# Performance work log

Hardware: AMD Instinct MI355X
Metric: run time of the kernel (lower is better)

Reference implementation:

```python
import jax, jax.numpy as jnp
import numpy as np
import math

B, S, DIM = 2, 2048, 2048
H = 16
NOPE, ROPE = 96, 32
HD = 128          # head_dim = NOPE + ROPE
KVR, QR = 512, 1536


def _rope_tables():
    inv_freq = 1.0 / (10000.0 ** (np.arange(0, ROPE, 2, dtype=np.float32) / ROPE))  # [ROPE/2]
    t = np.arange(S, dtype=np.float32)
    freqs = np.outer(t, inv_freq)  # [S, ROPE/2]
    return jnp.asarray(np.cos(freqs)), jnp.asarray(np.sin(freqs))


def setup_inputs() -> dict:
    key = jax.random.key(0)
    ks = jax.random.split(key, 8)
    w = 0.02
    cos, sin = _rope_tables()
    return {
        "x": jax.random.normal(ks[0], (B, S, DIM), jnp.float32),
        "freqs_cos": cos,
        "freqs_sin": sin,
        "wq_down": jax.random.normal(ks[1], (DIM, QR), jnp.float32) * w,
        "wq_up": jax.random.normal(ks[2], (QR, H * HD), jnp.float32) * w,
        "wkv_down": jax.random.normal(ks[3], (DIM, KVR), jnp.float32) * w,
        "w_up_nope": jax.random.normal(ks[4], (KVR, H * NOPE), jnp.float32) * w,
        "w_up_rope": jax.random.normal(ks[5], (KVR, H * ROPE), jnp.float32) * w,
        "w_up_val": jax.random.normal(ks[6], (KVR, H * HD), jnp.float32) * w,
        "wo": jax.random.normal(ks[7], (H * HD, DIM), jnp.float32) * w,
    }


def _apply_rope(x, cos, sin):
    # x: [B, S, H, D_r]; cos/sin: [S, D_r/2]
    xr = x[..., 0::2]
    xi = x[..., 1::2]
    c = cos[None, :, None, :]
    s = sin[None, :, None, :]
    out_r = xr * c - xi * s
    out_i = xr * s + xi * c
    return jnp.stack([out_r, out_i], axis=-1).reshape(x.shape)


def reference(x, freqs_cos, freqs_sin, wq_down, wq_up, wkv_down,
              w_up_nope, w_up_rope, w_up_val, wo):
    b, s, _ = x.shape
    # Q path: low-rank down then up
    q = (x @ wq_down) @ wq_up                 # [B,S,H*HD]
    q = q.reshape(b, s, H, HD)
    q_nope, q_rope = q[..., :NOPE], q[..., NOPE:]
    q_rope = _apply_rope(q_rope, freqs_cos, freqs_sin)

    # KV path: shared latent
    kv_latent = x @ wkv_down                  # [B,S,KVR]
    k_nope = (kv_latent @ w_up_nope).reshape(b, s, H, NOPE)
    k_rope = _apply_rope((kv_latent @ w_up_rope).reshape(b, s, H, ROPE),
                         freqs_cos, freqs_sin)
    v = (kv_latent @ w_up_val).reshape(b, s, H, HD)

    q_final = jnp.concatenate([q_nope, q_rope], axis=-1)   # [B,S,H,HD]
    k_final = jnp.concatenate([k_nope, k_rope], axis=-1)

    scores = jnp.einsum("bqhd,bkhd->bhqk", q_final, k_final) / math.sqrt(HD)
    causal = jnp.tril(jnp.ones((s, s), dtype=bool))        # [S,S]
    scores = jnp.where(causal[None, None], scores, -jnp.inf)
    attn = jax.nn.softmax(scores, axis=-1)
    out = jnp.einsum("bhqk,bkhd->bqhd", attn, v).reshape(b, s, H * HD)
    return out @ wo
```

## Files before the change

### kernel.cpp

```cpp
#include <hip/hip_runtime.h>
#include <hip/hip_bf16.h>
#include <stdint.h>

#define B_    2
#define S_    2048
#define DIM_  2048
#define H_    16
#define NOPE_ 96
#define ROPE_ 32
#define HD_   128
#define KVR_  512
#define QR_   1536
#define BS_   (B_*S_)
#define NQT_  (S_/128)

typedef __bf16 bf16_t;
typedef bf16_t bf16x8 __attribute__((ext_vector_type(8)));
typedef float  f32x4  __attribute__((ext_vector_type(4)));

__device__ __forceinline__ uint16_t f2bf(float f) {
  union { float f; uint32_t u; } v; v.f = f;
  uint32_t r = (v.u + 0x7fffu + ((v.u >> 16) & 1u)) >> 16;
  return (uint16_t)r;
}
__device__ __forceinline__ float bf2f(uint16_t h) {
  union { uint32_t u; float f; } v; v.u = ((uint32_t)h) << 16;
  return v.f;
}
__device__ __forceinline__ uint32_t pk_bf16(float a, float b) {
  union { float f; uint32_t u; } x, y; x.f = a; y.f = b;
  uint32_t lo = (x.u + 0x7fffu + ((x.u >> 16) & 1u)) >> 16;
  uint32_t hi = (y.u + 0x7fffu + ((y.u >> 16) & 1u)) & 0xffff0000u;
  return hi | lo;
}

__device__ __forceinline__ void gl_lds16(const void* g, void* l) {
  __builtin_amdgcn_global_load_lds(
      (const __attribute__((address_space(1))) uint32_t*)g,
      (__attribute__((address_space(3))) uint32_t*)l, 16, 0, 0);
}

__device__ __forceinline__ void transpose_tile(const float* __restrict__ W,
                                               uint16_t* __restrict__ Wt,
                                               int K, int N, float scale, int lbid,
                                               float (*tile)[65]) {
  const int nb = N / 64;
  const int n0 = (lbid % nb) * 64, k0 = (lbid / nb) * 64;
  const int tid = threadIdx.x;
  #pragma unroll
  for (int i = 0; i < 4; i++) {
    int p = i * 256 + tid;
    int r = p >> 4, c4 = (p & 15) * 4;
    float4 v = *(const float4*)&W[(size_t)(k0 + r) * N + n0 + c4];
    tile[r][c4 + 0] = v.x; tile[r][c4 + 1] = v.y; tile[r][c4 + 2] = v.z; tile[r][c4 + 3] = v.w;
  }
  __syncthreads();
  #pragma unroll
  for (int i = 0; i < 4; i++) {
    int p = i * 256 + tid;
    int rn = p >> 4, c4 = (p & 15) * 4;
    ushort4 o;
    o.x = f2bf(tile[c4 + 0][rn] * scale); o.y = f2bf(tile[c4 + 1][rn] * scale);
    o.z = f2bf(tile[c4 + 2][rn] * scale); o.w = f2bf(tile[c4 + 3][rn] * scale);
    *(ushort4*)&Wt[(size_t)(n0 + rn) * K + k0 + c4] = o;
  }
}

#define CAST_BLKS 2048
__global__ __launch_bounds__(256) void prep_k(
    const float* __restrict__ x,
    const float* __restrict__ wqd, const float* __restrict__ wqu,
    const float* __restrict__ wkvd, const float* __restrict__ wn,
    const float* __restrict__ wr, const float* __restrict__ wv,
    const float* __restrict__ wo,
    uint16_t* __restrict__ xb, uint16_t* __restrict__ wdT,
    uint16_t* __restrict__ wquT, uint16_t* __restrict__ wkrT,
    uint16_t* __restrict__ wvT, uint16_t* __restrict__ woT, float qscale) {
  __shared__ __align__(16) float tile[64][65];
  int bid = blockIdx.x;
  const int tid = threadIdx.x;
  if (bid < CAST_BLKS) {
    #pragma unroll
    for (int p = 0; p < 4; p++) {
      int i = bid * 4096 + p * 1024 + tid * 4;
      float4 v = *(const float4*)&x[i];
      ushort4 o; o.x = f2bf(v.x); o.y = f2bf(v.y); o.z = f2bf(v.z); o.w = f2bf(v.w);
      *(ushort4*)&xb[i] = o;
    }
    return;
  }
  bid -= CAST_BLKS;
  if (bid < 768)               transpose_tile(wqd,  wdT,                        2048, 1536, 1.f,    bid, tile);
  else if ((bid -= 768) < 256) transpose_tile(wkvd, wdT + (size_t)QR_ * DIM_,   2048,  512, 1.f,    bid, tile);
  else if ((bid -= 256) < 768) transpose_tile(wqu,  wquT,                       1536, 2048, qscale, bid, tile);
  else if ((bid -= 768) < 192) transpose_tile(wn,   wkrT,                        512, 1536, 1.f,    bid, tile);
  else if ((bid -= 192) < 64)  transpose_tile(wr,   wkrT + (size_t)1536 * 512,   512,  512, 1.f,    bid, tile);
  else if ((bid -= 64) < 256)  transpose_tile(wv,   wvT,                         512, 2048, 1.f,    bid, tile);
  else                         transpose_tile(wo,   woT, 2048, 2048, 1.f, bid - 256, tile);
}
#define PREP_BLKS (CAST_BLKS + 768 + 256 + 768 + 192 + 64 + 256 + 1024)

template<int MODE>
__global__ __launch_bounds__(256) void gemm_bt(const uint16_t* __restrict__ A,
                                               const uint16_t* __restrict__ Bt,
                                               void* __restrict__ C,
                                               int M, int N, int K,
                                               int lda, int ldb, int ldc,
                                               const float* __restrict__ cos_t,
                                               const float* __restrict__ sin_t) {
  __shared__ __align__(16) uint16_t As[128][64];
  __shared__ __align__(16) uint16_t Bs[128][64];
  const int tid = threadIdx.x;
  const int wave = tid >> 6, lane = tid & 63;
  const int wm = wave & 1, wn = wave >> 1;
  const int m0 = blockIdx.y * 128, n0 = blockIdx.x * 128;
  const int fr = lane & 15, fq = lane >> 4;

  f32x4 acc[4][4] = {};

  const int srow = wave * 32 + (lane >> 3);
  const int sg   = ((lane & 7) ^ ((lane >> 3) & 7));
  const int scol = sg * 8;

  for (int k0 = 0; k0 < K; k0 += 64) {
    #pragma unroll
    for (int i = 0; i < 4; i++) {
      gl_lds16(A  + (size_t)(m0 + srow + i * 8) * lda + k0 + scol, &As[wave * 32 + i * 8][0]);
      gl_lds16(Bt + (size_t)(n0 + srow + i * 8) * ldb + k0 + scol, &Bs[wave * 32 + i * 8][0]);
    }
    __syncthreads();
    #pragma unroll
    for (int ks = 0; ks < 2; ks++) {
      bf16x8 af[4], bf[4];
      #pragma unroll
      for (int mt = 0; mt < 4; mt++) {
        int pc = (ks * 4 + fq) ^ (fr & 7);
        af[mt] = *(const bf16x8*)&As[wm * 64 + mt * 16 + fr][pc * 8];
      }
      #pragma unroll
      for (int nt = 0; nt < 4; nt++) {
        int pc = (ks * 4 + fq) ^ (fr & 7);
        bf[nt] = *(const bf16x8*)&Bs[wn * 64 + nt * 16 + fr][pc * 8];
      }
      #pragma unroll
      for (int mt = 0; mt < 4; mt++)
        #pragma unroll
        for (int nt = 0; nt < 4; nt++)
          acc[mt][nt] = __builtin_amdgcn_mfma_f32_16x16x32_bf16(af[mt], bf[nt], acc[mt][nt], 0, 0, 0);
    }
    __syncthreads();
  }
  #pragma unroll
  for (int mt = 0; mt < 4; mt++) {
    #pragma unroll
    for (int nt = 0; nt < 4; nt++) {
      #pragma unroll
      for (int r = 0; r < 4; r++) {
        int gm = m0 + wm * 64 + mt * 16 + fq * 4 + r;
        int gn = n0 + wn * 64 + nt * 16 + fr;
        float v = acc[mt][nt][r];
        if (MODE == 0) {
          ((uint16_t*)C)[(size_t)gm * ldc + gn] = f2bf(v);
        } else if (MODE == 1) {
          ((float*)C)[(size_t)gm * ldc + gn] = v;
        } else if (MODE == 2) {
          float other = __shfl_xor(v, 1);
          int d = gn & 127;
          if (d >= 96) {
            int s = gm & (S_ - 1);
            int i = (d - 96) >> 1;
            float c = cos_t[s * 16 + i], sn = sin_t[s * 16 + i];
            v = (fr & 1) ? (other * sn + v * c) : (v * c - other * sn);
          }
          ((uint16_t*)C)[(size_t)gm * ldc + gn] = f2bf(v);
        } else {
          float other = __shfl_xor(v, 1);
          int dstcol;
          if (gn < 1536) {
            int h = gn / 96;
            dstcol = h * 128 + (gn - h * 96);
          } else {
            int ln = gn - 1536;
            int h = ln >> 5, dd = ln & 31;
            int s = gm & (S_ - 1);
            float c = cos_t[s * 16 + (dd >> 1)], sn = sin_t[s * 16 + (dd >> 1)];
            v = (fr & 1) ? (other * sn + v * c) : (v * c - other * sn);
            dstcol = h * 128 + 96 + dd;
          }
          ((uint16_t*)C)[(size_t)gm * 2048 + dstcol] = f2bf(v);
        }
      }
    }
  }
}

__global__ __launch_bounds__(512) void attn_kernel(const uint16_t* __restrict__ Q,
                                                   const uint16_t* __restrict__ Kf,
                                                   const uint16_t* __restrict__ Vt,
                                                   uint16_t* __restrict__ O) {
  __shared__ __align__(16) uint16_t Ks[64][128];
  __shared__ __align__(16) uint16_t Vs[128][64];
  __shared__ __align__(16) uint16_t Ps[8][16][72];
  const int bid = blockIdx.x;
  const int qt = (NQT_ - 1) - (bid / (H_ * B_));
  const int hb = bid % (H_ * B_);
  const int h = hb >> 1, b = hb & 1;
  const int tid = threadIdx.x, wave = tid >> 6, lane = tid & 63;
  const int fr = lane & 15, fq = lane >> 4;
  const int q0 = qt * 128;
  const int qrow = q0 + wave * 16;

  bf16x8 qf[4];
  const uint16_t* qbase = Q + (size_t)(b * S_ + qrow + fr) * (H_ * HD_) + h * HD_ + fq * 8;
  #pragma unroll
  for (int s4 = 0; s4 < 4; s4++) qf[s4] = *(const bf16x8*)(qbase + s4 * 32);

  float l_s = 0.f;
  f32x4 oacc[8] = {};

  const int ksrow_lo = wave * 4 + (lane >> 4);
  const int kg_chunk0 = (lane & 15);
  const int vsrow_lo = wave * 8 + (lane >> 3);
  const int vg_chunk = (lane & 7) ^ ((lane >> 3) & 7);

  const int nkt = 2 * qt + 2;
  for (int kt = 0; kt < nkt; kt++) {
    #pragma unroll
    for (int i = 0; i < 2; i++) {
      int row = i * 32 + ksrow_lo;
      int g = kg_chunk0 ^ (row & 15);
      gl_lds16(Kf + (size_t)(b * S_ + kt * 64 + row) * (H_ * HD_) + h * HD_ + g * 8,
               &Ks[i * 32 + wave * 4][0]);
    }
    #pragma unroll
    for (int i = 0; i < 2; i++) {
      int row = i * 64 + vsrow_lo;
      gl_lds16(Vt + (size_t)(h * HD_ + row) * BS_ + b * S_ + kt * 64 + vg_chunk * 8,
               &Vs[i * 64 + wave * 8][0]);
    }
    __syncthreads();

    if (kt * 64 <= qrow + 15) {
      f32x4 sacc[4] = {};
      #pragma unroll
      for (int ks = 0; ks < 4; ks++) {
        int pc = (ks * 4 + fq) ^ fr;
        #pragma unroll
        for (int nt = 0; nt < 4; nt++) {
          bf16x8 kfr = *(const bf16x8*)&Ks[nt * 16 + fr][pc * 8];
          sacc[nt] = __builtin_amdgcn_mfma_f32_16x16x32_bf16(kfr, qf[ks], sacc[nt], 0, 0, 0);
        }
      }
      const bool need_mask = (kt * 64 + 63 > qrow);
      const int qg = qrow + fr;
      #pragma unroll
      for (int nt = 0; nt < 4; nt++) {
        float p[4];
        #pragma unroll
        for (int r = 0; r < 4; r++) {
          float pp = __expf(sacc[nt][r]);
          if (need_mask) {
            int kg = kt * 64 + nt * 16 + fq * 4 + r;
            if (kg > qg) pp = 0.f;
          }
          l_s += pp;
          p[r] = pp;
        }
        uint2 w; w.x = pk_bf16(p[0], p[1]); w.y = pk_bf16(p[2], p[3]);
        *(uint2*)&Ps[wave][fr][nt * 16 + fq * 4] = w;
      }
      #pragma unroll
      for (int ks = 0; ks < 2; ks++) {
        bf16x8 pf = *(const bf16x8*)&Ps[wave][fr][ks * 32 + fq * 8];
        int pc = (ks * 4 + fq) ^ (fr & 7);
        #pragma unroll
        for (int d = 0; d < 8; d++) {
          bf16x8 vf = *(const bf16x8*)&Vs[d * 16 + fr][pc * 8];
          oacc[d] = __builtin_amdgcn_mfma_f32_16x16x32_bf16(vf, pf, oacc[d], 0, 0, 0);
        }
      }
    }
    __syncthreads();
  }
  l_s += __shfl_xor(l_s, 16);
  l_s += __shfl_xor(l_s, 32);
  const float inv_l = 1.0f / l_s;
  const int gm = b * S_ + qrow + fr;
  #pragma unroll
  for (int dt = 0; dt < 8; dt++) {
    ushort4 o;
    o.x = f2bf(oacc[dt][0] * inv_l); o.y = f2bf(oacc[dt][1] * inv_l);
    o.z = f2bf(oacc[dt][2] * inv_l); o.w = f2bf(oacc[dt][3] * inv_l);
    *(ushort4*)&O[(size_t)gm * (H_ * HD_) + h * HD_ + dt * 16 + fq * 4] = o;
  }
}

extern "C" void kernel_launch(void* const* d_in, const int* in_sizes, int n_in,
                              void* d_out, int out_size, void* d_ws, size_t ws_size,
                              hipStream_t stream) {
  const float* x        = (const float*)d_in[0];
  const float* fcos     = (const float*)d_in[1];
  const float* fsin     = (const float*)d_in[2];
  const float* wq_down  = (const float*)d_in[3];
  const float* wq_up    = (const float*)d_in[4];
  const float* wkv_down = (const float*)d_in[5];
  const float* w_nope   = (const float*)d_in[6];
  const float* w_rope   = (const float*)d_in[7];
  const float* w_val    = (const float*)d_in[8];
  const float* wo       = (const float*)d_in[9];
  float* out = (float*)d_out;

  char* ws = (char*)d_ws;
  size_t off = 0;
  auto alloc = [&](size_t elems) {
    uint16_t* p = (uint16_t*)(ws + off);
    off += elems * 2; off = (off + 255) & ~(size_t)255;
    return p;
  };
  uint16_t* xb     = alloc((size_t)BS_ * DIM_);
  uint16_t* wdT    = alloc((size_t)(QR_ + KVR_) * DIM_);
  uint16_t* wquT   = alloc((size_t)(H_ * HD_) * QR_);
  uint16_t* wkrT   = alloc((size_t)(H_ * NOPE_ + H_ * ROPE_) * KVR_);
  uint16_t* wvT    = alloc((size_t)(H_ * HD_) * KVR_);
  uint16_t* woT    = alloc((size_t)DIM_ * (H_ * HD_));
  uint16_t* latcat = alloc((size_t)BS_ * (QR_ + KVR_));
  uint16_t* qbuf   = alloc((size_t)BS_ * (H_ * HD_));
  uint16_t* kfin   = alloc((size_t)BS_ * (H_ * HD_));
  uint16_t* vTb    = alloc((size_t)(H_ * HD_) * BS_);
  uint16_t* aout   = alloc((size_t)BS_ * (H_ * HD_));

  const float qscale = 0.08838834764831845f;

  prep_k<<<dim3(PREP_BLKS), 256, 0, stream>>>(x, wq_down, wq_up, wkv_down, w_nope,
      w_rope, w_val, wo, xb, wdT, wquT, wkrT, wvT, woT, qscale);

  gemm_bt<0><<<dim3(2048 / 128, BS_ / 128), 256, 0, stream>>>(xb, wdT, latcat,
      BS_, 2048, DIM_, DIM_, DIM_, 2048, nullptr, nullptr);
  gemm_bt<2><<<dim3((H_ * HD_) / 128, BS_ / 128), 256, 0, stream>>>(latcat, wquT, qbuf,
      BS_, H_ * HD_, QR_, 2048, QR_, H_ * HD_, fcos, fsin);
  gemm_bt<3><<<dim3(2048 / 128, BS_ / 128), 256, 0, stream>>>(latcat + QR_, wkrT, kfin,
      BS_, 2048, KVR_, 2048, KVR_, 2048, fcos, fsin);
  gemm_bt<0><<<dim3(BS_ / 128, (H_ * HD_) / 128), 256, 0, stream>>>(wvT, latcat + QR_, vTb,
      H_ * HD_, BS_, KVR_, KVR_, 2048, BS_, nullptr, nullptr);

  attn_kernel<<<dim3(NQT_ * H_ * B_), 512, 0, stream>>>(qbuf, kfin, vTb, aout);
  gemm_bt<1><<<dim3(DIM_ / 128, BS_ / 128), 256, 0, stream>>>(aout, woT, out,
      BS_, DIM_, DIM_, DIM_, DIM_, DIM_, nullptr, nullptr);
}
```

Before: 371.6 us.

## Vectorize GEMM epilogue stores, use exp2 softmax, interleave attention tile order

```diff
diff --git a/kernel.cpp b/kernel.cpp
--- a/kernel.cpp
+++ b/kernel.cpp
@@ -22,10 +22,6 @@
   union { float f; uint32_t u; } v; v.f = f;
   uint32_t r = (v.u + 0x7fffu + ((v.u >> 16) & 1u)) >> 16;
   return (uint16_t)r;
-}
-__device__ __forceinline__ float bf2f(uint16_t h) {
-  union { uint32_t u; float f; } v; v.u = ((uint32_t)h) << 16;
-  return v.f;
 }
 __device__ __forceinline__ uint32_t pk_bf16(float a, float b) {
   union { float f; uint32_t u; } x, y; x.f = a; y.f = b;
@@ -146,49 +142,55 @@
       for (int mt = 0; mt < 4; mt++)
         #pragma unroll
         for (int nt = 0; nt < 4; nt++)
-          acc[mt][nt] = __builtin_amdgcn_mfma_f32_16x16x32_bf16(af[mt], bf[nt], acc[mt][nt], 0, 0, 0);
+          acc[mt][nt] = __builtin_amdgcn_mfma_f32_16x16x32_bf16(bf[nt], af[mt], acc[mt][nt], 0, 0, 0);
     }
     __syncthreads();
   }
   #pragma unroll
   for (int mt = 0; mt < 4; mt++) {
+    const int gm = m0 + wm * 64 + mt * 16 + fr;
     #pragma unroll
     for (int nt = 0; nt < 4; nt++) {
-      #pragma unroll
-      for (int r = 0; r < 4; r++) {
-        int gm = m0 + wm * 64 + mt * 16 + fq * 4 + r;
-        int gn = n0 + wn * 64 + nt * 16 + fr;
-        float v = acc[mt][nt][r];
-        if (MODE == 0) {
-          ((uint16_t*)C)[(size_t)gm * ldc + gn] = f2bf(v);
-        } else if (MODE == 1) {
-          ((float*)C)[(size_t)gm * ldc + gn] = v;
-        } else if (MODE == 2) {
-          float other = __shfl_xor(v, 1);
-          int d = gn & 127;
-          if (d >= 96) {
-            int s = gm & (S_ - 1);
-            int i = (d - 96) >> 1;
-            float c = cos_t[s * 16 + i], sn = sin_t[s * 16 + i];
-            v = (fr & 1) ? (other * sn + v * c) : (v * c - other * sn);
-          }
-          ((uint16_t*)C)[(size_t)gm * ldc + gn] = f2bf(v);
+      const int gn = n0 + wn * 64 + nt * 16 + fq * 4;
+      f32x4 a = acc[mt][nt];
+      if (MODE == 0) {
+        ushort4 o; o.x = f2bf(a[0]); o.y = f2bf(a[1]); o.z = f2bf(a[2]); o.w = f2bf(a[3]);
+        *(ushort4*)&((uint16_t*)C)[(size_t)gm * ldc + gn] = o;
+      } else if (MODE == 1) {
+        float4 o; o.x = a[0]; o.y = a[1]; o.z = a[2]; o.w = a[3];
+        *(float4*)&((float*)C)[(size_t)gm * ldc + gn] = o;
+      } else if (MODE == 2) {
+        int d = gn & 127;
+        if (d >= 96) {
+          int s = gm & (S_ - 1);
+          int i0 = (d - 96) >> 1;
+          float c0 = cos_t[s * 16 + i0],     s0 = sin_t[s * 16 + i0];
+          float c1 = cos_t[s * 16 + i0 + 1], s1 = sin_t[s * 16 + i0 + 1];
+          float r0 = a[0] * c0 - a[1] * s0, r1 = a[0] * s0 + a[1] * c0;
+          float r2 = a[2] * c1 - a[3] * s1, r3 = a[2] * s1 + a[3] * c1;
+          a[0] = r0; a[1] = r1; a[2] = r2; a[3] = r3;
+        }
+        ushort4 o; o.x = f2bf(a[0]); o.y = f2bf(a[1]); o.z = f2bf(a[2]); o.w = f2bf(a[3]);
+        *(ushort4*)&((uint16_t*)C)[(size_t)gm * ldc + gn] = o;
+      } else {
+        int dstcol;
+        if (gn < 1536) {
+          int h = gn / 96;
+          dstcol = h * 128 + (gn - h * 96);
         } else {
-          float other = __shfl_xor(v, 1);
-          int dstcol;
-          if (gn < 1536) {
-            int h = gn / 96;
-            dstcol = h * 128 + (gn - h * 96);
-          } else {
-            int ln = gn - 1536;
-            int h = ln >> 5, dd = ln & 31;
-            int s = gm & (S_ - 1);
-            float c = cos_t[s * 16 + (dd >> 1)], sn = sin_t[s * 16 + (dd >> 1)];
-            v = (fr & 1) ? (other * sn + v * c) : (v * c - other * sn);
-            dstcol = h * 128 + 96 + dd;
-          }
-          ((uint16_t*)C)[(size_t)gm * 2048 + dstcol] = f2bf(v);
-        }
+          int ln = gn - 1536;
+          int h = ln >> 5, dd = ln & 31;
+          int s = gm & (S_ - 1);
+          int i0 = dd >> 1;
+          float c0 = cos_t[s * 16 + i0],     s0 = sin_t[s * 16 + i0];
+          float c1 = cos_t[s * 16 + i0 + 1], s1 = sin_t[s * 16 + i0 + 1];
+          float r0 = a[0] * c0 - a[1] * s0, r1 = a[0] * s0 + a[1] * c0;
+          float r2 = a[2] * c1 - a[3] * s1, r3 = a[2] * s1 + a[3] * c1;
+          a[0] = r0; a[1] = r1; a[2] = r2; a[3] = r3;
+          dstcol = h * 128 + 96 + dd;
+        }
+        ushort4 o; o.x = f2bf(a[0]); o.y = f2bf(a[1]); o.z = f2bf(a[2]); o.w = f2bf(a[3]);
+        *(ushort4*)&((uint16_t*)C)[(size_t)gm * 2048 + dstcol] = o;
       }
     }
   }
@@ -202,8 +204,9 @@
   __shared__ __align__(16) uint16_t Vs[128][64];
   __shared__ __align__(16) uint16_t Ps[8][16][72];
   const int bid = blockIdx.x;
-  const int qt = (NQT_ - 1) - (bid / (H_ * B_));
-  const int hb = bid % (H_ * B_);
+  const int idx = bid & 255;
+  const int qt = (bid >> 8) ? (idx >> 5) : (NQT_ - 1 - (idx >> 5));
+  const int hb = idx & 31;
   const int h = hb >> 1, b = hb & 1;
   const int tid = threadIdx.x, wave = tid >> 6, lane = tid & 63;
   const int fr = lane & 15, fq = lane >> 4;
@@ -258,7 +261,7 @@
         float p[4];
         #pragma unroll
         for (int r = 0; r < 4; r++) {
-          float pp = __expf(sacc[nt][r]);
+          float pp = __builtin_amdgcn_exp2f(sacc[nt][r]);
           if (need_mask) {
             int kg = kt * 64 + nt * 16 + fq * 4 + r;
             if (kg > qg) pp = 0.f;
@@ -329,7 +332,7 @@
   uint16_t* vTb    = alloc((size_t)(H_ * HD_) * BS_);
   uint16_t* aout   = alloc((size_t)BS_ * (H_ * HD_));
 
-  const float qscale = 0.08838834764831845f;
+  const float qscale = 0.12751743f;
 
   prep_k<<<dim3(PREP_BLKS), 256, 0, stream>>>(x, wq_down, wq_up, wkv_down, w_nope,
       w_rope, w_val, wo, xb, wdT, wquT, wkrT, wvT, woT, qscale);
```

After: 374.6 us. About the same (+0.8%).
